# Performance work log

Measured on AMD Instinct MI355X. Metric: run time of the kernel, lower is better.

## Reference

```python
import jax, jax.numpy as jnp
import numpy as np

T, D, K = 8192, 1024, 1024
LMBDA = 5.0
BIG = jnp.float32(3.0e38)  # finite stand-in for +inf so (f - lmbda) stays finite


def setup_inputs() -> dict:
    key = jax.random.key(0)
    k1, k2 = jax.random.split(key)
    return {
        "features": jax.random.normal(k1, (T, D), dtype=jnp.float32),
        "codebook": jax.random.normal(k2, (K, D), dtype=jnp.float32),
    }


def _dpdp(features, codebook, lmbda):
    # squared euclidean distances, (T, K)
    d2 = (
        jnp.sum(features * features, axis=1, keepdims=True)
        - 2.0 * features @ codebook.T
        + jnp.sum(codebook * codebook, axis=1)
    )
    Tn = features.shape[0]
    Kn = codebook.shape[0]

    # Incremental O(T*K) form of the original O(T^2*K) recurrence:
    # f_t[k] = min_{s<=t-1} alpha[s] - lmbda*(t-1-s) + sum_{i=s..t-1} d2[i,k]
    #        = d2[t-1,k] + min(alpha[t-1], f_{t-1}[k] - lmbda)
    # alpha[t] = min_k f_t[k]; beta[t] = start index s of argmin; gamma[t] = argmin_k.
    def fwd_step(carry, inp):
        f, s, alpha = carry  # f:(K,), s:(K,) segment start per codeword, alpha: scalar
        d_t, t = inp
        ext = f - lmbda                      # extend existing segment
        take_new = alpha < ext               # start a new segment at t
        f_new = d_t + jnp.minimum(alpha, ext)
        s_new = jnp.where(take_new, t, s)
        k_star = jnp.argmin(f_new)
        alpha_new = f_new[k_star]
        return (f_new, s_new, alpha_new), (s_new[k_star], k_star.astype(jnp.int32))

    init = (jnp.full((Kn,), BIG, jnp.float32), jnp.zeros((Kn,), jnp.int32), jnp.float32(0.0))
    ts = jnp.arange(Tn, dtype=jnp.int32)
    _, (betas, gammas) = jax.lax.scan(fwd_step, init, (d2, ts))
    # betas[t-1]/gammas[t-1] correspond to alpha index t in the original code.

    # Backtrack: units[beta[cur]:cur] = gamma[cur]; cur = beta[cur].
    def bwd_step(cur, p):
        g = gammas[cur - 1]
        b = betas[cur - 1]
        cur_new = jnp.where(p == b, p, cur)
        return cur_new, g

    _, units = jax.lax.scan(bwd_step, jnp.int32(Tn), ts, reverse=True)
    return units


def reference(features, codebook):
    units = _dpdp(features, codebook, LMBDA)
    quantized = codebook[units]
    quantized_st = features - jax.lax.stop_gradient(features - quantized)
    return quantized_st, units
```

## Files before the change

### kernel.cpp

```cpp
#include <hip/hip_runtime.h>
#include <hip/hip_bf16.h>
#include <stdint.h>

#define T_N 8192
#define K_N 1024
#define D_N 1024
#define LMBDA 5.0f
#define BIGF 3.0e38f
#define CMAX 32
#define THR 26.0f
#define QNAN 0x7FC00000

__global__ __launch_bounds__(256) void k_norms(const float* __restrict__ F,
                                               const float* __restrict__ C,
                                               float* __restrict__ sf2,
                                               float* __restrict__ sc2) {
#pragma clang fp contract(off)
  int wave = threadIdx.x >> 6;
  int lane = threadIdx.x & 63;
  int row = blockIdx.x * 4 + wave;
  const float* src;
  float* dst;
  if (row < T_N) { src = F + (size_t)row * D_N; dst = sf2 + row; }
  else           { src = C + (size_t)(row - T_N) * D_N; dst = sc2 + (row - T_N); }
  int leaf = lane >> 3, j = lane & 7;
  const float* p = src + leaf * 128 + j;
  float x = p[0];
  float r = x * x;
#pragma unroll
  for (int i = 1; i < 16; ++i) {
    float y = p[8 * i];
    r = r + y * y;
  }
  r = r + __shfl_xor(r, 1, 64);
  r = r + __shfl_xor(r, 2, 64);
  r = r + __shfl_xor(r, 4, 64);
  r = r + __shfl_xor(r, 8, 64);
  r = r + __shfl_xor(r, 16, 64);
  r = r + __shfl_xor(r, 32, 64);
  if (lane == 0) *dst = r;
}

__global__ __launch_bounds__(256) void k_gemm(const float* __restrict__ F,
                                              const float* __restrict__ C,
                                              const float* __restrict__ sf2,
                                              const float* __restrict__ sc2,
                                              float* __restrict__ d2) {
  __shared__ float As[32][68];
  __shared__ float Bs[32][68];
  int t0 = (int)(blockIdx.x >> 4) * 64;
  int k0 = (int)(blockIdx.x & 15) * 64;
  int tid = threadIdx.x;
  int tx = tid & 15, ty = tid >> 4;
  float acc[4][4], p0[4][4], p1[4][4];
#pragma unroll
  for (int i = 0; i < 4; ++i)
#pragma unroll
    for (int j = 0; j < 4; ++j) { acc[i][j] = 0.0f; p0[i][j] = 0.0f; p1[i][j] = 0.0f; }
  int r = tid & 63;
  int cbase = (tid >> 6) * 2;
  for (int d0 = 0; d0 < D_N; d0 += 32) {
    __syncthreads();
#pragma unroll
    for (int p = 0; p < 2; ++p) {
      int c4 = cbase + p;
      float4 va = *(const float4*)&F[(size_t)(t0 + r) * D_N + d0 + c4 * 4];
      As[c4 * 4 + 0][r] = va.x; As[c4 * 4 + 1][r] = va.y;
      As[c4 * 4 + 2][r] = va.z; As[c4 * 4 + 3][r] = va.w;
      float4 vb = *(const float4*)&C[(size_t)(k0 + r) * D_N + d0 + c4 * 4];
      Bs[c4 * 4 + 0][r] = vb.x; Bs[c4 * 4 + 1][r] = vb.y;
      Bs[c4 * 4 + 2][r] = vb.z; Bs[c4 * 4 + 3][r] = vb.w;
    }
    __syncthreads();
#pragma unroll
    for (int d = 0; d < 32; ++d) {
      float4 a = *(const float4*)&As[d][ty * 4];
      float4 b = *(const float4*)&Bs[d][tx * 4];
      acc[0][0] = fmaf(a.x, b.x, acc[0][0]); acc[0][1] = fmaf(a.x, b.y, acc[0][1]);
      acc[0][2] = fmaf(a.x, b.z, acc[0][2]); acc[0][3] = fmaf(a.x, b.w, acc[0][3]);
      acc[1][0] = fmaf(a.y, b.x, acc[1][0]); acc[1][1] = fmaf(a.y, b.y, acc[1][1]);
      acc[1][2] = fmaf(a.y, b.z, acc[1][2]); acc[1][3] = fmaf(a.y, b.w, acc[1][3]);
      acc[2][0] = fmaf(a.z, b.x, acc[2][0]); acc[2][1] = fmaf(a.z, b.y, acc[2][1]);
      acc[2][2] = fmaf(a.z, b.z, acc[2][2]); acc[2][3] = fmaf(a.z, b.w, acc[2][3]);
      acc[3][0] = fmaf(a.w, b.x, acc[3][0]); acc[3][1] = fmaf(a.w, b.y, acc[3][1]);
      acc[3][2] = fmaf(a.w, b.z, acc[3][2]); acc[3][3] = fmaf(a.w, b.w, acc[3][3]);
    }
    if (d0 == 352) {
#pragma unroll
      for (int i = 0; i < 4; ++i)
#pragma unroll
        for (int j = 0; j < 4; ++j) { p0[i][j] = acc[i][j]; acc[i][j] = 0.0f; }
    }
    if (d0 == 736) {
#pragma unroll
      for (int i = 0; i < 4; ++i)
#pragma unroll
        for (int j = 0; j < 4; ++j) { p1[i][j] = acc[i][j]; acc[i][j] = 0.0f; }
    }
  }
  {
#pragma clang fp contract(off)
#pragma unroll
    for (int i = 0; i < 4; ++i) {
      int t = t0 + ty * 4 + i;
      float sa = sf2[t];
      float o[4];
#pragma unroll
      for (int j = 0; j < 4; ++j) {
        float dot = (p0[i][j] + p1[i][j]) + acc[i][j];
        float two = 2.0f * dot;
        o[j] = (sa - two) + sc2[k0 + tx * 4 + j];
      }
      float4 ov; ov.x = o[0]; ov.y = o[1]; ov.z = o[2]; ov.w = o[3];
      *(float4*)&d2[(size_t)t * K_N + k0 + tx * 4] = ov;
    }
  }
}

__global__ __launch_bounds__(256) void k_cand(const float* __restrict__ d2,
                                              int2* __restrict__ cand,
                                              float* __restrict__ dminOut) {
  int wave = threadIdx.x >> 6;
  int lane = threadIdx.x & 63;
  int row = blockIdx.x * 4 + wave;
  const float4* p = (const float4*)(d2 + (size_t)row * K_N + lane * 16);
  float4 v0 = p[0], v1 = p[1], v2 = p[2], v3 = p[3];
  float m = fminf(fminf(fminf(v0.x, v0.y), fminf(v0.z, v0.w)),
                  fminf(fminf(v1.x, v1.y), fminf(v1.z, v1.w)));
  float n = fminf(fminf(fminf(v2.x, v2.y), fminf(v2.z, v2.w)),
                  fminf(fminf(v3.x, v3.y), fminf(v3.z, v3.w)));
  m = fminf(m, n);
  m = fminf(m, __shfl_xor(m, 1, 64));
  m = fminf(m, __shfl_xor(m, 2, 64));
  m = fminf(m, __shfl_xor(m, 4, 64));
  m = fminf(m, __shfl_xor(m, 8, 64));
  m = fminf(m, __shfl_xor(m, 16, 64));
  m = fminf(m, __shfl_xor(m, 32, 64));
  if (lane == 0) dminOut[row] = m;
  float thr = m + THR;
  unsigned flags = 0;
#define TESTC(J, VAL) if ((VAL) <= thr) flags |= (1u << (J));
  TESTC(0, v0.x) TESTC(1, v0.y) TESTC(2, v0.z) TESTC(3, v0.w)
  TESTC(4, v1.x) TESTC(5, v1.y) TESTC(6, v1.z) TESTC(7, v1.w)
  TESTC(8, v2.x) TESTC(9, v2.y) TESTC(10, v2.z) TESTC(11, v2.w)
  TESTC(12, v3.x) TESTC(13, v3.y) TESTC(14, v3.z) TESTC(15, v3.w)
#undef TESTC
  int c = __popc(flags);
  int pre = c;
#pragma unroll
  for (int off = 1; off <= 32; off <<= 1) {
    int t = __shfl_up(pre, off, 64);
    if (lane >= off) pre += t;
  }
  int idx = pre - c;
  int2* rowp = cand + (size_t)row * CMAX;
  int kb = lane * 16;
#define EMITC(J, VAL)                                                        \
  if (flags & (1u << (J))) {                                                 \
    if (idx < CMAX) rowp[idx] = make_int2(kb + (J), __float_as_int(VAL));    \
    ++idx;                                                                   \
  }
  EMITC(0, v0.x) EMITC(1, v0.y) EMITC(2, v0.z) EMITC(3, v0.w)
  EMITC(4, v1.x) EMITC(5, v1.y) EMITC(6, v1.z) EMITC(7, v1.w)
  EMITC(8, v2.x) EMITC(9, v2.y) EMITC(10, v2.z) EMITC(11, v2.w)
  EMITC(12, v3.x) EMITC(13, v3.y) EMITC(14, v3.z) EMITC(15, v3.w)
#undef EMITC
}

__global__ __launch_bounds__(256) void k_prev2(const int2* __restrict__ cand,
                                               int4* __restrict__ pairbuf) {
  __shared__ int km1k[4][32];
  __shared__ int km1d[4][32];
  __shared__ int kt0k[4][32];
  __shared__ int kt0d[4][32];
  int w = threadIdx.x >> 6, lane = threadIdx.x & 63;
  int p = blockIdx.x * 4 + w;
  int t0 = 2 * p, t1 = 2 * p + 1, tm1 = t0 - 1;
  if (lane < 32) {
    int2 c0 = cand[(size_t)t0 * CMAX + lane];
    kt0k[w][lane] = c0.x; kt0d[w][lane] = c0.y;
  } else {
    int j = lane - 32;
    int2 cm = (p > 0) ? cand[(size_t)tm1 * CMAX + j] : make_int2(-2, 0);
    km1k[w][j] = cm.x; km1d[w][j] = cm.y;
  }
  __syncthreads();
  int4 out;
  if (lane < 32) {
    int2 c1 = cand[(size_t)t1 * CMAX + lane];
    int k1 = c1.x;
    int pp2 = -4, d0 = QNAN, d1s = 0;
    bool in0 = false;
#pragma unroll
    for (int i = 0; i < 32; ++i) if (kt0k[w][i] == k1) { d0 = kt0d[w][i]; in0 = true; }
#pragma unroll
    for (int i = 0; i < 32; ++i) if (km1k[w][i] == k1) { pp2 = i * 4; d1s = km1d[w][i]; }
    if (!in0 || k1 < 0) { pp2 = -4; d0 = QNAN; }
    out = make_int4(pp2, d0, d1s, 0);
  } else {
    int i0 = lane - 32;
    int k0 = kt0k[w][i0];
    int d0 = kt0d[w][i0];
    int pp = -4, d1s = 0;
#pragma unroll
    for (int i = 0; i < 32; ++i) if (km1k[w][i] == k0) { pp = i * 4; d1s = km1d[w][i]; }
    if (k0 < 0) pp = -4;
    out = make_int4(pp, d0, d1s, 0);
  }
  pairbuf[(size_t)p * 64 + lane] = out;
}

__device__ __forceinline__ float dpp_min32(float x) {
  int t;
  t = __builtin_amdgcn_update_dpp(__float_as_int(x), __float_as_int(x), 0x111, 0xF, 0xF, false);
  x = fminf(x, __int_as_float(t));
  t = __builtin_amdgcn_update_dpp(__float_as_int(x), __float_as_int(x), 0x112, 0xF, 0xF, false);
  x = fminf(x, __int_as_float(t));
  t = __builtin_amdgcn_update_dpp(__float_as_int(x), __float_as_int(x), 0x114, 0xF, 0xF, false);
  x = fminf(x, __int_as_float(t));
  t = __builtin_amdgcn_update_dpp(__float_as_int(x), __float_as_int(x), 0x118, 0xF, 0xF, false);
  x = fminf(x, __int_as_float(t));
  t = __builtin_amdgcn_update_dpp(__float_as_int(x), __float_as_int(x), 0x142, 0xF, 0xF, false);
  x = fminf(x, __int_as_float(t));
  return x;
}
__device__ __forceinline__ float rdlane(float x, int l) {
  return __int_as_float(__builtin_amdgcn_readlane(__float_as_int(x), l));
}

__global__ __launch_bounds__(64, 1) void k_pass1(const int4* __restrict__ pairbuf,
                                                 const int2* __restrict__ cand,
                                                 const float* __restrict__ dminArr,
                                                 float* __restrict__ alphaOut) {
  const int lane = threadIdx.x;
  const int4* basep = pairbuf + lane;
  const int2* basec = cand + (lane & 31);
  int4 rg[8];
  int2 rgc[8];
#pragma unroll
  for (int u = 0; u < 8; ++u) {
    rg[u] = basep[(size_t)u * 64];
    rgc[u] = basec[(size_t)(2 * u + 1) * CMAX];
  }
  float mabprev = BIGF;
  float alpha = 0.0f;
  float redAB = 0.0f;
  float dmT1prev = 0.0f;
  float areg = 0.0f;
  float dmv_next = dminArr[lane];
  const int NP = T_N / 2;
  for (int pb32 = 0; pb32 < NP; pb32 += 32) {
    float dmv = dmv_next;
    int nb = pb32 + 32; if (nb >= NP) nb = 0;
    dmv_next = dminArr[2 * nb + lane];
    for (int pb8 = 0; pb8 < 32; pb8 += 8) {
#pragma unroll
      for (int u = 0; u < 8; ++u) {
        int p = pb32 + pb8 + u;
        int4 pv = rg[u];
        int2 cv = rgc[u];
        float aEnter = alpha;
        int g1 = __builtin_amdgcn_ds_bpermute(pv.x, __float_as_int(mabprev));
        int pn = p + 8; if (pn > NP - 1) pn = NP - 1;
        rg[u] = basep[(size_t)pn * 64];
        rgc[u] = basec[(size_t)(2 * pn + 1) * CMAX];
        float Pab = rdlane(redAB, 31);
        alpha = fminf(Pab, dmT1prev + aEnter);
        int posA = 2 * p - 1;
        if (posA >= 0) {
          areg = ((posA & 63) == lane) ? alpha : areg;
          if ((posA & 63) == 63) alphaOut[(posA & ~63) + lane] = areg;
        }
        int r0 = 2 * (pb8 + u);
        float dm0 = rdlane(dmv, r0);
        float dm1 = rdlane(dmv, r0 + 1);
        float inj = __int_as_float(pv.z) + aEnter;
        float fp = (pv.x < 0) ? BIGF : fminf(__int_as_float(g1), inj);
        float d0 = __int_as_float(pv.y);
        float d1 = __int_as_float(cv.y);
        float v0 = d0 + (fp - LMBDA);
        float A1 = d1 + (v0 - LMBDA);
        float B0 = d0 + alpha;
        float B1 = d1 + (B0 - LMBDA);
        float mab = fminf(A1, B1);
        float x = (lane < 32) ? mab : v0;
        float red = dpp_min32(x);
        float Pp0 = rdlane(red, 63);
        float a0 = fminf(Pp0, dm0 + alpha);
        areg = (((2 * p) & 63) == lane) ? a0 : areg;
        mabprev = mab;
        redAB = red;
        dmT1prev = dm1;
        alpha = a0;
      }
    }
  }
  float Pab = rdlane(redAB, 31);
  alpha = fminf(Pab, dmT1prev + alpha);
  areg = (lane == 63) ? alpha : areg;
  alphaOut[(T_N - 64) + lane] = areg;
}

#define CH 512
#define WARM 64
__global__ __launch_bounds__(256) void k_pass2(const float* __restrict__ d2,
                                               const float* __restrict__ AOUT,
                                               unsigned* __restrict__ pack) {
  int kb = blockIdx.x & 3;
  int tc = blockIdx.x >> 2;
  int k = kb * 256 + threadIdx.x;
  int ts = tc * CH;
  int start = ts - WARM; if (start < 0) start = 0;
  int end = ts + CH;
  __shared__ float lal[CH + WARM + 1];
  for (int i = threadIdx.x; i < end - start + 1; i += 256) {
    int idx = start - 1 + i;
    lal[i] = (idx < 0) ? 0.0f : AOUT[idx];
  }
  __syncthreads();
  float f = BIGF;
  unsigned s = 0;
#pragma unroll 4
  for (int tau = start; tau < end; ++tau) {
    float a_in = lal[tau - start];
    float d = d2[(size_t)tau * K_N + k];
    float ext = f - LMBDA;
    if (a_in < ext) s = (unsigned)tau;
    f = d + fminf(a_in, ext);
    if (tau >= ts) {
      float a_out = lal[tau - start + 1];
      if (f == a_out) atomicMin(&pack[tau], ((unsigned)k << 13) | s);
    }
  }
}

__global__ __launch_bounds__(256) void k_backtrack(const unsigned* __restrict__ pack,
                                                   unsigned* __restrict__ unitsWs,
                                                   float* __restrict__ outUnits) {
  __shared__ unsigned lp[T_N];
  __shared__ unsigned long long msk[T_N / 64];
  int tid = threadIdx.x;
  for (int i = tid * 4; i < T_N; i += 1024) {
    *(uint4*)&lp[i] = *(const uint4*)&pack[i];
  }
  __syncthreads();
  if (tid < 64) {
    int lane = tid;
    int cur = T_N;
    for (int B = T_N - 64; B >= 0; B -= 64) {
      unsigned long long marks = 0ull;
      if (cur > B) {
        unsigned pk = lp[B + lane];
        int bv = (int)(pk & 8191u);
        unsigned long long run = __ballot(bv == B + lane);
        while (cur > B) {
          int L = cur - 1 - B;
          unsigned long long below = (L == 63) ? ~0ull : ((1ull << (L + 1)) - 1ull);
          unsigned long long nz = (~run) & below;
          if (nz == 0ull) { marks |= below; cur = B; break; }
          int j = 63 - __builtin_clzll(nz);
          marks |= below & ~((1ull << j) - 1ull);
          int nb = __builtin_amdgcn_readlane(bv, j);
          cur = nb;
          if (cur > B + j) cur = B + j;
        }
      }
      if (lane == 0) msk[B >> 6] = marks;
    }
  }
  __syncthreads();
  for (int p = tid; p < T_N; p += 256) {
    int w = p >> 6;
    unsigned long long m = msk[w] & (~0ull << (p & 63));
    while (m == 0ull) { ++w; m = msk[w]; }
    int idx = (w << 6) + (int)__builtin_ctzll(m);
    unsigned g = (lp[idx] >> 13) & 1023u;
    unitsWs[p] = g;
    outUnits[p] = (float)g;
  }
}

__global__ __launch_bounds__(256) void k_gather(const float* __restrict__ C,
                                                const unsigned* __restrict__ unitsWs,
                                                float* __restrict__ out) {
  int t = blockIdx.x;
  unsigned u = unitsWs[t] & 1023u;
  const float4* src = (const float4*)(C + (size_t)u * D_N);
  float4* dst = (float4*)(out + (size_t)t * D_N);
  dst[threadIdx.x] = src[threadIdx.x];
}

extern "C" void kernel_launch(void* const* d_in, const int* in_sizes, int n_in,
                              void* d_out, int out_size, void* d_ws, size_t ws_size,
                              hipStream_t stream) {
  const float* F = (const float*)d_in[0];
  const float* C = (const float*)d_in[1];
  float* out = (float*)d_out;
  float* d2 = out;
  float* outUnits = out + (size_t)T_N * D_N;
  char* ws = (char*)d_ws;
  float* alphaOut = (float*)(ws);
  unsigned* pack = (unsigned*)(ws + (32 << 10));
  unsigned* unitsWs = (unsigned*)(ws + (64 << 10));
  float* sf2 = (float*)(ws + (96 << 10));
  float* sc2 = (float*)(ws + (128 << 10));
  float* dminArr = (float*)(ws + (160 << 10));
  int2* cand = (int2*)(ws + (1 << 20));
  int4* pairbuf = (int4*)(ws + (3 << 20));

  k_norms<<<(T_N + K_N) / 4, 256, 0, stream>>>(F, C, sf2, sc2);
  hipMemsetAsync(pack, 0xFF, T_N * sizeof(unsigned), stream);
  hipMemsetAsync(cand, 0xFF, (size_t)T_N * CMAX * sizeof(int2), stream);
  k_gemm<<<(T_N / 64) * (K_N / 64), 256, 0, stream>>>(F, C, sf2, sc2, d2);
  k_cand<<<T_N / 4, 256, 0, stream>>>(d2, cand, dminArr);
  k_prev2<<<(T_N / 2) / 4, 256, 0, stream>>>(cand, pairbuf);
  k_pass1<<<1, 64, 0, stream>>>(pairbuf, cand, dminArr, alphaOut);
  k_pass2<<<(T_N / CH) * 4, 256, 0, stream>>>(d2, alphaOut, pack);
  k_backtrack<<<1, 256, 0, stream>>>(pack, unitsWs, outUnits);
  k_gather<<<T_N, 256, 0, stream>>>(C, unitsWs, out);
}
```

Baseline: 1.032 ms.

## Widen GEMM tile to 64x128 with 4x8 per-thread micro-tile; halve pass2 chunk

The distance GEMM now covers 64x128 output tiles per block, each thread computing a 4x8 register micro-tile. This raises FMA-per-LDS-load reuse and halves the number of A-tile reloads. The three split partial accumulators are folded into a running sum, which keeps the reduction order unchanged. The pass2 chunk size drops from 512 to 256, giving twice as many blocks for parallelism at the cost of more warm-up overlap work. The main risks are higher register pressure lowering occupancy and fewer GEMM blocks.

```diff
diff --git a/kernel.cpp b/kernel.cpp
--- a/kernel.cpp
+++ b/kernel.cpp
@@ -47,55 +47,61 @@
                                               const float* __restrict__ sc2,
                                               float* __restrict__ d2) {
   __shared__ float As[32][68];
-  __shared__ float Bs[32][68];
-  int t0 = (int)(blockIdx.x >> 4) * 64;
-  int k0 = (int)(blockIdx.x & 15) * 64;
+  __shared__ float Bs[32][132];
+  int t0 = (int)(blockIdx.x >> 3) * 64;
+  int k0 = (int)(blockIdx.x & 7) * 128;
   int tid = threadIdx.x;
   int tx = tid & 15, ty = tid >> 4;
-  float acc[4][4], p0[4][4], p1[4][4];
+  float dot[4][8], acc[4][8];
 #pragma unroll
   for (int i = 0; i < 4; ++i)
 #pragma unroll
-    for (int j = 0; j < 4; ++j) { acc[i][j] = 0.0f; p0[i][j] = 0.0f; p1[i][j] = 0.0f; }
-  int r = tid & 63;
-  int cbase = (tid >> 6) * 2;
+    for (int j = 0; j < 8; ++j) { dot[i][j] = 0.0f; acc[i][j] = 0.0f; }
+  int ra = tid & 63, ca = (tid >> 6) * 8;
+  int rb = tid & 127, cb = (tid >> 7) * 16;
   for (int d0 = 0; d0 < D_N; d0 += 32) {
     __syncthreads();
-#pragma unroll
-    for (int p = 0; p < 2; ++p) {
-      int c4 = cbase + p;
-      float4 va = *(const float4*)&F[(size_t)(t0 + r) * D_N + d0 + c4 * 4];
-      As[c4 * 4 + 0][r] = va.x; As[c4 * 4 + 1][r] = va.y;
-      As[c4 * 4 + 2][r] = va.z; As[c4 * 4 + 3][r] = va.w;
-      float4 vb = *(const float4*)&C[(size_t)(k0 + r) * D_N + d0 + c4 * 4];
-      Bs[c4 * 4 + 0][r] = vb.x; Bs[c4 * 4 + 1][r] = vb.y;
-      Bs[c4 * 4 + 2][r] = vb.z; Bs[c4 * 4 + 3][r] = vb.w;
+    {
+      const float* fa = &F[(size_t)(t0 + ra) * D_N + d0 + ca];
+      float4 a0 = *(const float4*)fa;
+      float4 a1 = *(const float4*)(fa + 4);
+      As[ca + 0][ra] = a0.x; As[ca + 1][ra] = a0.y; As[ca + 2][ra] = a0.z; As[ca + 3][ra] = a0.w;
+      As[ca + 4][ra] = a1.x; As[ca + 5][ra] = a1.y; As[ca + 6][ra] = a1.z; As[ca + 7][ra] = a1.w;
+      const float* fb = &C[(size_t)(k0 + rb) * D_N + d0 + cb];
+      float4 b0 = *(const float4*)fb;
+      float4 b1 = *(const float4*)(fb + 4);
+      float4 b2 = *(const float4*)(fb + 8);
+      float4 b3 = *(const float4*)(fb + 12);
+      Bs[cb + 0][rb] = b0.x; Bs[cb + 1][rb] = b0.y; Bs[cb + 2][rb] = b0.z; Bs[cb + 3][rb] = b0.w;
+      Bs[cb + 4][rb] = b1.x; Bs[cb + 5][rb] = b1.y; Bs[cb + 6][rb] = b1.z; Bs[cb + 7][rb] = b1.w;
+      Bs[cb + 8][rb] = b2.x; Bs[cb + 9][rb] = b2.y; Bs[cb + 10][rb] = b2.z; Bs[cb + 11][rb] = b2.w;
+      Bs[cb + 12][rb] = b3.x; Bs[cb + 13][rb] = b3.y; Bs[cb + 14][rb] = b3.z; Bs[cb + 15][rb] = b3.w;
     }
     __syncthreads();
 #pragma unroll
     for (int d = 0; d < 32; ++d) {
       float4 a = *(const float4*)&As[d][ty * 4];
-      float4 b = *(const float4*)&Bs[d][tx * 4];
-      acc[0][0] = fmaf(a.x, b.x, acc[0][0]); acc[0][1] = fmaf(a.x, b.y, acc[0][1]);
-      acc[0][2] = fmaf(a.x, b.z, acc[0][2]); acc[0][3] = fmaf(a.x, b.w, acc[0][3]);
-      acc[1][0] = fmaf(a.y, b.x, acc[1][0]); acc[1][1] = fmaf(a.y, b.y, acc[1][1]);
-      acc[1][2] = fmaf(a.y, b.z, acc[1][2]); acc[1][3] = fmaf(a.y, b.w, acc[1][3]);
-      acc[2][0] = fmaf(a.z, b.x, acc[2][0]); acc[2][1] = fmaf(a.z, b.y, acc[2][1]);
-      acc[2][2] = fmaf(a.z, b.z, acc[2][2]); acc[2][3] = fmaf(a.z, b.w, acc[2][3]);
-      acc[3][0] = fmaf(a.w, b.x, acc[3][0]); acc[3][1] = fmaf(a.w, b.y, acc[3][1]);
-      acc[3][2] = fmaf(a.w, b.z, acc[3][2]); acc[3][3] = fmaf(a.w, b.w, acc[3][3]);
+      float4 b0 = *(const float4*)&Bs[d][tx * 8];
+      float4 b1 = *(const float4*)&Bs[d][tx * 8 + 4];
+      float av[4] = {a.x, a.y, a.z, a.w};
+      float bv[8] = {b0.x, b0.y, b0.z, b0.w, b1.x, b1.y, b1.z, b1.w};
+#pragma unroll
+      for (int i = 0; i < 4; ++i)
+#pragma unroll
+        for (int j = 0; j < 8; ++j)
+          acc[i][j] = fmaf(av[i], bv[j], acc[i][j]);
     }
     if (d0 == 352) {
 #pragma unroll
       for (int i = 0; i < 4; ++i)
 #pragma unroll
-        for (int j = 0; j < 4; ++j) { p0[i][j] = acc[i][j]; acc[i][j] = 0.0f; }
+        for (int j = 0; j < 8; ++j) { dot[i][j] = acc[i][j]; acc[i][j] = 0.0f; }
     }
     if (d0 == 736) {
 #pragma unroll
       for (int i = 0; i < 4; ++i)
 #pragma unroll
-        for (int j = 0; j < 4; ++j) { p1[i][j] = acc[i][j]; acc[i][j] = 0.0f; }
+        for (int j = 0; j < 8; ++j) { dot[i][j] = dot[i][j] + acc[i][j]; acc[i][j] = 0.0f; }
     }
   }
   {
@@ -104,15 +110,18 @@
     for (int i = 0; i < 4; ++i) {
       int t = t0 + ty * 4 + i;
       float sa = sf2[t];
-      float o[4];
-#pragma unroll
-      for (int j = 0; j < 4; ++j) {
-        float dot = (p0[i][j] + p1[i][j]) + acc[i][j];
-        float two = 2.0f * dot;
-        o[j] = (sa - two) + sc2[k0 + tx * 4 + j];
+      float o[8];
+#pragma unroll
+      for (int j = 0; j < 8; ++j) {
+        float dsum = dot[i][j] + acc[i][j];
+        float two = 2.0f * dsum;
+        o[j] = (sa - two) + sc2[k0 + tx * 8 + j];
       }
-      float4 ov; ov.x = o[0]; ov.y = o[1]; ov.z = o[2]; ov.w = o[3];
-      *(float4*)&d2[(size_t)t * K_N + k0 + tx * 4] = ov;
+      float4 o0; o0.x = o[0]; o0.y = o[1]; o0.z = o[2]; o0.w = o[3];
+      float4 o1; o1.x = o[4]; o1.y = o[5]; o1.z = o[6]; o1.w = o[7];
+      float* dp = &d2[(size_t)t * K_N + k0 + tx * 8];
+      *(float4*)dp = o0;
+      *(float4*)(dp + 4) = o1;
     }
   }
 }
@@ -301,7 +310,7 @@
   alphaOut[(T_N - 64) + lane] = areg;
 }
 
-#define CH 512
+#define CH 256
 #define WARM 64
 __global__ __launch_bounds__(256) void k_pass2(const float* __restrict__ d2,
                                                const float* __restrict__ AOUT,
@@ -411,7 +420,7 @@
   k_norms<<<(T_N + K_N) / 4, 256, 0, stream>>>(F, C, sf2, sc2);
   hipMemsetAsync(pack, 0xFF, T_N * sizeof(unsigned), stream);
   hipMemsetAsync(cand, 0xFF, (size_t)T_N * CMAX * sizeof(int2), stream);
-  k_gemm<<<(T_N / 64) * (K_N / 64), 256, 0, stream>>>(F, C, sf2, sc2, d2);
+  k_gemm<<<(T_N / 64) * (K_N / 128), 256, 0, stream>>>(F, C, sf2, sc2, d2);
   k_cand<<<T_N / 4, 256, 0, stream>>>(d2, cand, dminArr);
   k_prev2<<<(T_N / 2) / 4, 256, 0, stream>>>(cand, pairbuf);
   k_pass1<<<1, 64, 0, stream>>>(pairbuf, cand, dminArr, alphaOut);
```

Measured after the change: 951.5 us. 7.8% less time.
